# Kernel optimization log

Measured on AMD Instinct MI355X. Metric: run time of the kernel, lower is better.

The kernel has to match this reference:

```python
import jax, jax.numpy as jnp
import numpy as np

B, S, HID = 2, 2048, 4096
NH, NKV, HD = 32, 8, 128
N_REP = NH // NKV
SCALING = HD ** -0.5


def rotate_half(x):
    x1, x2 = x[..., : x.shape[-1] // 2], x[..., x.shape[-1] // 2 :]
    return jnp.concatenate((-x2, x1), axis=-1)


def setup_inputs() -> dict:
    key = jax.random.key(0)
    ks = jax.random.split(key, 8)
    hidden_states = jax.random.normal(ks[0], (B, S, HID), dtype=jnp.float32)
    # rotary embeddings (realistic cos/sin from inverse-frequency angles)
    inv_freq = 1.0 / (10000.0 ** (jnp.arange(0, HD, 2, dtype=jnp.float32) / HD))
    pos = jnp.arange(S, dtype=jnp.float32)
    ang = pos[:, None] * inv_freq[None, :]  # [S, HD/2]
    emb = jnp.concatenate([ang, ang], axis=-1)  # [S, HD]
    cos = jnp.broadcast_to(jnp.cos(emb)[None], (B, S, HD))
    sin = jnp.broadcast_to(jnp.sin(emb)[None], (B, S, HD))
    # additive causal mask [B,1,S,S]
    causal = jnp.triu(jnp.full((S, S), -1e9, dtype=jnp.float32), k=1)
    attention_mask = jnp.broadcast_to(causal[None, None], (B, 1, S, S))
    std = HID ** -0.5
    Wq = jax.random.normal(ks[1], (NH * HD, HID), dtype=jnp.float32) * std
    Wk = jax.random.normal(ks[2], (NKV * HD, HID), dtype=jnp.float32) * std
    Wv = jax.random.normal(ks[3], (NKV * HD, HID), dtype=jnp.float32) * std
    Wo = jax.random.normal(ks[4], (HID, NH * HD), dtype=jnp.float32) * std
    return {"hidden_states": hidden_states, "cos": cos, "sin": sin,
            "attention_mask": attention_mask, "Wq": Wq, "Wk": Wk, "Wv": Wv, "Wo": Wo}


def reference(hidden_states, cos, sin, attention_mask, Wq, Wk, Wv, Wo):
    b, s, _ = hidden_states.shape
    # projections (nn.Linear: x @ W.T), reshape to [B, H, S, D]
    q = (hidden_states @ Wq.T).reshape(b, s, NH, HD).transpose(0, 2, 1, 3)
    k = (hidden_states @ Wk.T).reshape(b, s, NKV, HD).transpose(0, 2, 1, 3)
    v = (hidden_states @ Wv.T).reshape(b, s, NKV, HD).transpose(0, 2, 1, 3)
    # RoPE, cos/sin broadcast over head dim
    c, sn = cos[:, None], sin[:, None]  # [B,1,S,D]
    q = q * c + rotate_half(q) * sn
    k = k * c + rotate_half(k) * sn
    # GQA repeat_kv
    k = jnp.repeat(k, N_REP, axis=1)
    v = jnp.repeat(v, N_REP, axis=1)
    # eager attention
    attn = jnp.einsum("bhqd,bhkd->bhqk", q, k) * SCALING
    attn = attn + attention_mask[:, :, :, : k.shape[2]]
    attn = jax.nn.softmax(attn.astype(jnp.float32), axis=-1).astype(q.dtype)
    out = jnp.einsum("bhqk,bhkd->bhqd", attn, v)
    out = out.transpose(0, 2, 1, 3).reshape(b, s, NH * HD)
    return out @ Wo.T
```

## Files before the change

### kernel.cpp

```cpp
#include <hip/hip_runtime.h>


typedef __bf16 bf16x8 __attribute__((ext_vector_type(8)));
typedef __bf16 bf16x4 __attribute__((ext_vector_type(4)));
typedef float floatx4 __attribute__((ext_vector_type(4)));

#define S_LEN 2048
#define HIDN  4096
#define NH    32
#define NKV   8
#define HD    128

__device__ inline void async_copy16(const void* g, void* l) {
  __builtin_amdgcn_global_load_lds(
      (const __attribute__((address_space(1))) void*)g,
      (__attribute__((address_space(3))) void*)l, 16, 0, 0);
}

template<int N> __device__ __forceinline__ void waitv() {
  static_assert(N == 0 || N == 3 || N == 4 || N == 6 || N == 8, "vmcnt");
  if constexpr (N == 0)      asm volatile("s_waitcnt vmcnt(0)" ::: "memory");
  else if constexpr (N == 3) asm volatile("s_waitcnt vmcnt(3)" ::: "memory");
  else if constexpr (N == 4) asm volatile("s_waitcnt vmcnt(4)" ::: "memory");
  else if constexpr (N == 6) asm volatile("s_waitcnt vmcnt(6)" ::: "memory");
  else                       asm volatile("s_waitcnt vmcnt(8)" ::: "memory");
}

__global__ __launch_bounds__(256) void cvt_bf16(const float* __restrict__ src,
                                                __bf16* __restrict__ dst, int n8)
{
  int i = blockIdx.x * 256 + threadIdx.x;
  if (i >= n8) return;
  const float4* s = (const float4*)src + (size_t)i * 2;
  float4 a = s[0], b = s[1];
  bf16x8 r = {(__bf16)a.x, (__bf16)a.y, (__bf16)a.z, (__bf16)a.w,
              (__bf16)b.x, (__bf16)b.y, (__bf16)b.z, (__bf16)b.w};
  *((bf16x8*)dst + i) = r;
}

template<int MI_REP>
__device__ __forceinline__ void gemm_core(
    const __bf16* __restrict__ A, const __bf16* __restrict__ WB,
    __bf16* lds, int m0, int n0, int tid, floatx4 (&acc)[MI_REP][4])
{
  constexpr int BM       = MI_REP * 32;
  constexpr int A_BYTES  = BM * 64;
  constexpr int STAGE_B  = A_BYTES + 256 * 64;
  constexpr int A_ROUNDS = BM / 128;
  constexpr int LPT      = A_ROUNDS + 2;
  constexpr int NK       = HIDN / 32;

  const int wave = tid >> 6, lane = tid & 63;
  const int quad = lane >> 4, l16 = lane & 15;
  const int wm = wave >> 2, wn = wave & 3;

  size_t a_src[A_ROUNDS], b_src[2];
  #pragma unroll
  for (int ra = 0; ra < A_ROUNDS; ra++) {
    int idx = ra * 512 + tid;
    int row = idx >> 2, qlog = (idx & 3) ^ ((idx >> 3) & 3);
    a_src[ra] = (size_t)(m0 + row) * HIDN + qlog * 8;
  }
  #pragma unroll
  for (int rb = 0; rb < 2; rb++) {
    int idx = rb * 512 + tid;
    int row = idx >> 2, qlog = (idx & 3) ^ ((idx >> 3) & 3);
    b_src[rb] = (size_t)(n0 + row) * HIDN + qlog * 8;
  }
  const int sw   = (quad ^ ((l16 >> 1) & 3)) * 16;
  const int a_rd = (wm * (MI_REP * 16) + l16) * 64 + sw;
  const int b_rd = A_BYTES + (wn * 64 + l16) * 64 + sw;

  #pragma unroll
  for (int mi = 0; mi < MI_REP; mi++)
    #pragma unroll
    for (int ni = 0; ni < 4; ni++) acc[mi][ni] = (floatx4){0.f, 0.f, 0.f, 0.f};

  char* ldsb = (char*)lds;
  auto stage = [&](int kt) {
    char* sb = ldsb + (size_t)(kt & 3) * STAGE_B;
    const __bf16* ak = A  + (size_t)kt * 32;
    const __bf16* bk = WB + (size_t)kt * 32;
    #pragma unroll
    for (int ra = 0; ra < A_ROUNDS; ra++)
      async_copy16(ak + a_src[ra], sb + (ra * 512 + tid) * 16);
    #pragma unroll
    for (int rb = 0; rb < 2; rb++)
      async_copy16(bk + b_src[rb], sb + A_BYTES + (rb * 512 + tid) * 16);
  };

  stage(0); stage(1); stage(2);

  #pragma unroll 4
  for (int kt = 0; kt < NK; kt++) {
    if (kt < NK - 2)       waitv<2 * LPT>();
    else if (kt == NK - 2) waitv<LPT>();
    else                   waitv<0>();
    __builtin_amdgcn_s_barrier();
    asm volatile("" ::: "memory");
    if (kt + 3 < NK) stage(kt + 3);

    const char* sb = ldsb + (size_t)(kt & 3) * STAGE_B;
    bf16x8 bv[4], av[MI_REP];
    #pragma unroll
    for (int ni = 0; ni < 4; ni++)
      bv[ni] = *(const bf16x8*)(sb + b_rd + ni * 1024);
    #pragma unroll
    for (int mi = 0; mi < MI_REP; mi++)
      av[mi] = *(const bf16x8*)(sb + a_rd + mi * 1024);

    __builtin_amdgcn_s_setprio(1);
    #pragma unroll
    for (int mi = 0; mi < MI_REP; mi++)
      #pragma unroll
      for (int ni = 0; ni < 4; ni++)
        acc[mi][ni] = __builtin_amdgcn_mfma_f32_16x16x32_bf16(
            bv[ni], av[mi], acc[mi][ni], 0, 0, 0);
    __builtin_amdgcn_s_setprio(0);
  }
}

__global__ __launch_bounds__(512, 2) void qkv_gemm_bf16(
    const __bf16* __restrict__ A, const __bf16* __restrict__ WB,
    __bf16* __restrict__ Qb, __bf16* __restrict__ Kb, __bf16* __restrict__ Vt)
{
  __shared__ __bf16 lds[4 * (128 + 256) * 32];
  const int tid = threadIdx.x;
  const int m0 = blockIdx.y * 128, n0 = blockIdx.x * 256;
  floatx4 acc[4][4];
  gemm_core<4>(A, WB, lds, m0, n0, tid, acc);

  const int wave = tid >> 6, lane = tid & 63;
  const int quad = lane >> 4, l16 = lane & 15;
  const int wm = wave >> 2, wn = wave & 3;
  #pragma unroll
  for (int mi = 0; mi < 4; mi++) {
    int m = m0 + wm * 64 + mi * 16 + l16;
    int b = m >> 11, s = m & (S_LEN - 1);
    #pragma unroll
    for (int ni = 0; ni < 4; ni++) {
      int nb = n0 + wn * 64 + ni * 16 + quad * 4;
      if (nb < 4096) {
        int hh = nb >> 7, d = nb & 127;
        bf16x4 v = {(__bf16)acc[mi][ni][0], (__bf16)acc[mi][ni][1],
                    (__bf16)acc[mi][ni][2], (__bf16)acc[mi][ni][3]};
        *(bf16x4*)&Qb[(((size_t)b * NH + hh) * S_LEN + s) * HD + d] = v;
      } else if (nb < 5120) {
        int nl = nb - 4096, hh = nl >> 7, d = nl & 127;
        bf16x4 v = {(__bf16)acc[mi][ni][0], (__bf16)acc[mi][ni][1],
                    (__bf16)acc[mi][ni][2], (__bf16)acc[mi][ni][3]};
        *(bf16x4*)&Kb[(((size_t)b * NKV + hh) * S_LEN + s) * HD + d] = v;
      } else {
        int nl = nb - 5120, hh = nl >> 7, d = nl & 127;
        #pragma unroll
        for (int r = 0; r < 4; r++)
          Vt[(((size_t)b * NKV + hh) * HD + d + r) * S_LEN + s] =
              (__bf16)acc[mi][ni][r];
      }
    }
  }
}

__global__ __launch_bounds__(512, 2) void out_gemm_bf16(
    const __bf16* __restrict__ A, const __bf16* __restrict__ WB,
    float* __restrict__ C)
{
  __shared__ __bf16 lds[4 * (256 + 256) * 32];
  const int tid = threadIdx.x;
  const int m0 = blockIdx.y * 256, n0 = blockIdx.x * 256;
  floatx4 acc[8][4];
  gemm_core<8>(A, WB, lds, m0, n0, tid, acc);

  const int wave = tid >> 6, lane = tid & 63;
  const int quad = lane >> 4, l16 = lane & 15;
  const int wm = wave >> 2, wn = wave & 3;
  #pragma unroll
  for (int mi = 0; mi < 8; mi++) {
    int m = m0 + wm * 128 + mi * 16 + l16;
    #pragma unroll
    for (int ni = 0; ni < 4; ni++) {
      int nb = n0 + wn * 64 + ni * 16 + quad * 4;
      *(floatx4*)&C[(size_t)m * HIDN + nb] = acc[mi][ni];
    }
  }
}

__global__ __launch_bounds__(256) void qkv_gemm_f32(
    const float* __restrict__ A, const float* __restrict__ Wq,
    const float* __restrict__ Wk, const float* __restrict__ Wv,
    __bf16* __restrict__ Qb, __bf16* __restrict__ Kb, __bf16* __restrict__ Vt)
{
  __shared__ __bf16 As[128 * 40];
  __shared__ __bf16 Bs[128 * 40];
  const int tid  = threadIdx.x;
  const int wave = tid >> 6, lane = tid & 63;
  const int quad = lane >> 4, l16 = lane & 15;
  const int wrow = (wave >> 1) * 64, wcol = (wave & 1) * 64;
  const int m0 = blockIdx.y * 128;
  const int n0 = blockIdx.x * 128;

  const float* W; int wr0; int sel;
  if (n0 < 4096)      { W = Wq; wr0 = n0;        sel = 0; }
  else if (n0 < 5120) { W = Wk; wr0 = n0 - 4096; sel = 1; }
  else                { W = Wv; wr0 = n0 - 5120; sel = 2; }

  floatx4 acc[4][4];
  #pragma unroll
  for (int i = 0; i < 4; i++)
    #pragma unroll
    for (int j = 0; j < 4; j++) acc[i][j] = (floatx4){0.f, 0.f, 0.f, 0.f};

  for (int k0 = 0; k0 < HIDN; k0 += 32) {
    __syncthreads();
    #pragma unroll
    for (int it = 0; it < 4; ++it) {
      int c = tid + it * 256;
      int row = c >> 3, c4 = (c & 7) * 4;
      float4 va = *(const float4*)(A + (size_t)(m0 + row) * HIDN + k0 + c4);
      __bf16* da = &As[row * 40 + c4];
      da[0] = (__bf16)va.x; da[1] = (__bf16)va.y; da[2] = (__bf16)va.z; da[3] = (__bf16)va.w;
      float4 vb = *(const float4*)(W + (size_t)(wr0 + row) * HIDN + k0 + c4);
      __bf16* db = &Bs[row * 40 + c4];
      db[0] = (__bf16)vb.x; db[1] = (__bf16)vb.y; db[2] = (__bf16)vb.z; db[3] = (__bf16)vb.w;
    }
    __syncthreads();
    bf16x8 af[4], bfr[4];
    #pragma unroll
    for (int i = 0; i < 4; i++)
      af[i] = *(const bf16x8*)&As[(wrow + i * 16 + l16) * 40 + quad * 8];
    #pragma unroll
    for (int j = 0; j < 4; j++)
      bfr[j] = *(const bf16x8*)&Bs[(wcol + j * 16 + l16) * 40 + quad * 8];
    #pragma unroll
    for (int i = 0; i < 4; i++)
      #pragma unroll
      for (int j = 0; j < 4; j++)
        acc[i][j] = __builtin_amdgcn_mfma_f32_16x16x32_bf16(af[i], bfr[j], acc[i][j], 0, 0, 0);
  }

  #pragma unroll
  for (int i = 0; i < 4; i++) {
    #pragma unroll
    for (int j = 0; j < 4; j++) {
      #pragma unroll
      for (int r = 0; r < 4; r++) {
        int m = m0 + wrow + i * 16 + quad * 4 + r;
        int n = n0 + wcol + j * 16 + l16;
        __bf16 v = (__bf16)acc[i][j][r];
        int b = m >> 11, s = m & (S_LEN - 1);
        if (sel == 0) {
          int h = n >> 7, d = n & 127;
          Qb[(((size_t)b * NH + h) * S_LEN + s) * HD + d] = v;
        } else if (sel == 1) {
          int nl = n - 4096, h = nl >> 7, d = nl & 127;
          Kb[(((size_t)b * NKV + h) * S_LEN + s) * HD + d] = v;
        } else {
          int nl = n - 5120, h = nl >> 7, d = nl & 127;
          Vt[(((size_t)b * NKV + h) * HD + d) * S_LEN + s] = v;
        }
      }
    }
  }
}

__global__ __launch_bounds__(256) void out_gemm_f32(
    const __bf16* __restrict__ A, const float* __restrict__ Wo,
    float* __restrict__ C)
{
  __shared__ __bf16 As[128 * 40];
  __shared__ __bf16 Bs[128 * 40];
  const int tid  = threadIdx.x;
  const int wave = tid >> 6, lane = tid & 63;
  const int quad = lane >> 4, l16 = lane & 15;
  const int wrow = (wave >> 1) * 64, wcol = (wave & 1) * 64;
  const int m0 = blockIdx.y * 128;
  const int n0 = blockIdx.x * 128;

  floatx4 acc[4][4];
  #pragma unroll
  for (int i = 0; i < 4; i++)
    #pragma unroll
    for (int j = 0; j < 4; j++) acc[i][j] = (floatx4){0.f, 0.f, 0.f, 0.f};

  for (int k0 = 0; k0 < HIDN; k0 += 32) {
    __syncthreads();
    #pragma unroll
    for (int it = 0; it < 2; ++it) {
      int c = tid + it * 256;
      int row = c >> 2, c8 = (c & 3) * 8;
      *(bf16x8*)&As[row * 40 + c8] =
          *(const bf16x8*)(A + (size_t)(m0 + row) * HIDN + k0 + c8);
    }
    #pragma unroll
    for (int it = 0; it < 4; ++it) {
      int c = tid + it * 256;
      int row = c >> 3, c4 = (c & 7) * 4;
      float4 vb = *(const float4*)(Wo + (size_t)(n0 + row) * HIDN + k0 + c4);
      __bf16* db = &Bs[row * 40 + c4];
      db[0] = (__bf16)vb.x; db[1] = (__bf16)vb.y; db[2] = (__bf16)vb.z; db[3] = (__bf16)vb.w;
    }
    __syncthreads();
    bf16x8 af[4], bfr[4];
    #pragma unroll
    for (int i = 0; i < 4; i++)
      af[i] = *(const bf16x8*)&As[(wrow + i * 16 + l16) * 40 + quad * 8];
    #pragma unroll
    for (int j = 0; j < 4; j++)
      bfr[j] = *(const bf16x8*)&Bs[(wcol + j * 16 + l16) * 40 + quad * 8];
    #pragma unroll
    for (int i = 0; i < 4; i++)
      #pragma unroll
      for (int j = 0; j < 4; j++)
        acc[i][j] = __builtin_amdgcn_mfma_f32_16x16x32_bf16(af[i], bfr[j], acc[i][j], 0, 0, 0);
  }

  #pragma unroll
  for (int i = 0; i < 4; i++)
    #pragma unroll
    for (int j = 0; j < 4; j++)
      #pragma unroll
      for (int r = 0; r < 4; r++) {
        int m = m0 + wrow + i * 16 + quad * 4 + r;
        int n = n0 + wcol + j * 16 + l16;
        C[(size_t)m * HIDN + n] = acc[i][j][r];
      }
}

__global__ __launch_bounds__(256) void rope_kernel(
    __bf16* __restrict__ Qb, __bf16* __restrict__ Kb,
    const float* __restrict__ cosp, const float* __restrict__ sinp)
{
  size_t i = (size_t)blockIdx.x * 256 + threadIdx.x;
  const size_t QP = (size_t)2 * NH * S_LEN * 64;
  __bf16* buf; int H; size_t t;
  if (i < QP) { buf = Qb; H = NH;  t = i; }
  else        { buf = Kb; H = NKV; t = i - QP; }
  int d = (int)(t & 63);
  int s = (int)((t >> 6) & (S_LEN - 1));
  size_t rest = t >> 17;
  int h = (int)(rest % H);
  int b = (int)(rest / H);
  size_t base = (((size_t)b * H + h) * S_LEN + s) * HD;
  float q0 = (float)buf[base + d];
  float q1 = (float)buf[base + d + 64];
  float c  = cosp[((size_t)b * S_LEN + s) * HD + d];
  float sn = sinp[((size_t)b * S_LEN + s) * HD + d];
  buf[base + d]      = (__bf16)(q0 * c - q1 * sn);
  buf[base + d + 64] = (__bf16)(q1 * c + q0 * sn);
}

__global__ __launch_bounds__(256, 2) void flash_attn(
    const __bf16* __restrict__ Q, const __bf16* __restrict__ Kc,
    const __bf16* __restrict__ Vt, __bf16* __restrict__ Out)
{
  __shared__ __bf16 Ks[64 * 136];
  __shared__ __bf16 VTs[128 * 72];
  __shared__ __bf16 Ps[4 * 32 * 72];
  const int tid  = threadIdx.x;
  const int wave = tid >> 6, lane = tid & 63;
  const int quad = lane >> 4, l16 = lane & 15;
  const int bh = blockIdx.x;
  const int h = bh & 31, b = bh >> 5;
  const int qt = 15 - (int)blockIdx.y;
  const int kvh = h >> 2;
  const size_t qbase  = (((size_t)b * NH + h) * S_LEN + qt * 128 + wave * 32) * HD;
  const size_t kbase  = ((size_t)b * NKV + kvh) * S_LEN * HD;
  const size_t vtbase = ((size_t)b * NKV + kvh) * (size_t)HD * S_LEN;
  const int psbase = wave * (32 * 72);

  bf16x8 qf[2][4];
  #pragma unroll
  for (int st = 0; st < 2; st++)
    #pragma unroll
    for (int kk = 0; kk < 4; kk++)
      qf[st][kk] = *(const bf16x8*)&Q[qbase + (size_t)(st * 16 + l16) * HD + kk * 32 + quad * 8];

  floatx4 o[2][8];
  floatx4 ol[2];
  #pragma unroll
  for (int st = 0; st < 2; st++) {
    ol[st] = (floatx4){0.f, 0.f, 0.f, 0.f};
    #pragma unroll
    for (int ct = 0; ct < 8; ct++) o[st][ct] = (floatx4){0.f, 0.f, 0.f, 0.f};
  }
  bf16x8 onesv;
  #pragma unroll
  for (int u = 0; u < 8; u++) onesv[u] = (__bf16)1.0f;

  const float c1 = 0.12753785f;
  const float c2 = -28.853900f;
  const int kj_end = 2 * qt + 2;

  bf16x8 kreg[4], vreg[4];
  #pragma unroll
  for (int it = 0; it < 4; ++it) {
    int c = tid + it * 256;
    kreg[it] = *(const bf16x8*)&Kc[kbase + (size_t)((c >> 4)) * HD + (c & 15) * 8];
    vreg[it] = *(const bf16x8*)&Vt[vtbase + (size_t)(c >> 3) * S_LEN + (c & 7) * 8];
  }

  for (int kj = 0; kj < kj_end; ++kj) {
    __syncthreads();
    #pragma unroll
    for (int it = 0; it < 4; ++it) {
      int c = tid + it * 256;
      *(bf16x8*)&Ks[(c >> 4) * 136 + (c & 15) * 8] = kreg[it];
      *(bf16x8*)&VTs[(c >> 3) * 72 + (c & 7) * 8] = vreg[it];
    }
    __syncthreads();

    if (kj + 1 < kj_end) {
      #pragma unroll
      for (int it = 0; it < 4; ++it) {
        int c = tid + it * 256;
        kreg[it] = *(const bf16x8*)&Kc[kbase + (size_t)((kj + 1) * 64 + (c >> 4)) * HD + (c & 15) * 8];
        vreg[it] = *(const bf16x8*)&Vt[vtbase + (size_t)(c >> 3) * S_LEN + (kj + 1) * 64 + (c & 7) * 8];
      }
    }

    floatx4 s[2][4];
    #pragma unroll
    for (int st = 0; st < 2; st++)
      #pragma unroll
      for (int j = 0; j < 4; j++) s[st][j] = (floatx4){0.f, 0.f, 0.f, 0.f};
    #pragma unroll
    for (int kk = 0; kk < 4; kk++) {
      bf16x8 ak[4];
      #pragma unroll
      for (int j = 0; j < 4; j++)
        ak[j] = *(const bf16x8*)&Ks[(j * 16 + l16) * 136 + kk * 32 + quad * 8];
      #pragma unroll
      for (int st = 0; st < 2; st++)
        #pragma unroll
        for (int j = 0; j < 4; j++)
          s[st][j] = __builtin_amdgcn_mfma_f32_16x16x32_bf16(ak[j], qf[st][kk], s[st][j], 0, 0, 0);
    }

    #pragma unroll
    for (int st = 0; st < 2; st++) {
      const int qrow = qt * 128 + wave * 32 + st * 16 + l16;
      #pragma unroll
      for (int j = 0; j < 4; j++) {
        const int kvb = kj * 64 + j * 16 + quad * 4;
        bf16x4 pw;
        #pragma unroll
        for (int r = 0; r < 4; r++) {
          float p = __builtin_amdgcn_exp2f(fmaf(s[st][j][r], c1, c2));
          if (kvb + r > qrow) p = 0.0f;
          pw[r] = (__bf16)p;
        }
        *(bf16x4*)&Ps[psbase + (st * 16 + l16) * 72 + j * 16 + quad * 4] = pw;
      }
    }

    #pragma unroll
    for (int kk = 0; kk < 2; kk++) {
      bf16x8 bv[8];
      #pragma unroll
      for (int ct = 0; ct < 8; ct++)
        bv[ct] = *(const bf16x8*)&VTs[(ct * 16 + l16) * 72 + kk * 32 + quad * 8];
      #pragma unroll
      for (int st = 0; st < 2; st++) {
        bf16x8 ap = *(const bf16x8*)&Ps[psbase + (st * 16 + l16) * 72 + kk * 32 + quad * 8];
        ol[st] = __builtin_amdgcn_mfma_f32_16x16x32_bf16(ap, onesv, ol[st], 0, 0, 0);
        #pragma unroll
        for (int ct = 0; ct < 8; ct++)
          o[st][ct] = __builtin_amdgcn_mfma_f32_16x16x32_bf16(ap, bv[ct], o[st][ct], 0, 0, 0);
      }
    }
  }

  #pragma unroll
  for (int st = 0; st < 2; st++) {
    #pragma unroll
    for (int r = 0; r < 4; r++) {
      float rl = 1.0f / ol[st][r];
      int qi = qt * 128 + wave * 32 + st * 16 + quad * 4 + r;
      #pragma unroll
      for (int ct = 0; ct < 8; ct++) {
        Out[((size_t)b * S_LEN + qi) * HIDN + h * HD + ct * 16 + l16] =
            (__bf16)(o[st][ct][r] * rl);
      }
    }
  }
}

extern "C" void kernel_launch(void* const* d_in, const int* in_sizes, int n_in,
                              void* d_out, int out_size, void* d_ws, size_t ws_size,
                              hipStream_t stream)
{
  const float* hs   = (const float*)d_in[0];
  const float* cosp = (const float*)d_in[1];
  const float* sinp = (const float*)d_in[2];
  const float* Wq   = (const float*)d_in[4];
  const float* Wk   = (const float*)d_in[5];
  const float* Wv   = (const float*)d_in[6];
  const float* Wo   = (const float*)d_in[7];
  float* out = (float*)d_out;

  __bf16* Qb  = (__bf16*)d_ws;
  __bf16* Kb  = Qb  + (size_t)16777216;
  __bf16* Vtb = Kb  + (size_t)4194304;

  if (ws_size >= (size_t)134217728) {
    __bf16* HSB = Vtb + (size_t)4194304;
    __bf16* AO  = HSB;
    __bf16* WB  = HSB + (size_t)16777216;

    cvt_bf16<<<8192, 256, 0, stream>>>(hs, HSB, 2097152);
    cvt_bf16<<<8192, 256, 0, stream>>>(Wq, WB, 2097152);
    cvt_bf16<<<2048, 256, 0, stream>>>(Wk, WB + 16777216, 524288);
    cvt_bf16<<<2048, 256, 0, stream>>>(Wv, WB + 20971520, 524288);
    qkv_gemm_bf16<<<dim3(24, 32), 512, 0, stream>>>(HSB, WB, Qb, Kb, Vtb);
    cvt_bf16<<<8192, 256, 0, stream>>>(Wo, WB, 2097152);
    rope_kernel<<<40960, 256, 0, stream>>>(Qb, Kb, cosp, sinp);
    flash_attn<<<dim3(64, 16), 256, 0, stream>>>(Qb, Kb, Vtb, AO);
    out_gemm_bf16<<<dim3(16, 16), 512, 0, stream>>>(AO, WB, out);
  } else {
    __bf16* AO = Vtb + (size_t)4194304;
    qkv_gemm_f32<<<dim3(48, 32), 256, 0, stream>>>(hs, Wq, Wk, Wv, Qb, Kb, Vtb);
    rope_kernel<<<40960, 256, 0, stream>>>(Qb, Kb, cosp, sinp);
    flash_attn<<<dim3(64, 16), 256, 0, stream>>>(Qb, Kb, Vtb, AO);
    out_gemm_f32<<<dim3(32, 32), 256, 0, stream>>>(AO, Wo, out);
  }
}
```

Before: 672.9 us.

## Use BK=64 triple-buffered GEMM core, smaller out-proj tile, setprio in attention

Replaces the BK=32 four-stage GEMM core with a BK=64 three-stage ring buffer. It uses a new XOR swizzle over 8 chunks, and each barrier now covers twice as many MFMAs. The output projection switches from 256x256 tiles to 128x256, doubling its grid so more workgroups fill the CUs. The flash-attention inner loops hoist the P-fragment loads and wrap their MFMA blocks in s_setprio. The aim is fewer barriers and waits per unit of K and better occupancy, at the cost of more LDS per stage and less reuse per output-GEMM tile.

```diff
diff --git a/kernel.cpp b/kernel.cpp
--- a/kernel.cpp
+++ b/kernel.cpp
@@ -18,12 +18,9 @@
 }
 
 template<int N> __device__ __forceinline__ void waitv() {
-  static_assert(N == 0 || N == 3 || N == 4 || N == 6 || N == 8, "vmcnt");
-  if constexpr (N == 0)      asm volatile("s_waitcnt vmcnt(0)" ::: "memory");
-  else if constexpr (N == 3) asm volatile("s_waitcnt vmcnt(3)" ::: "memory");
-  else if constexpr (N == 4) asm volatile("s_waitcnt vmcnt(4)" ::: "memory");
-  else if constexpr (N == 6) asm volatile("s_waitcnt vmcnt(6)" ::: "memory");
-  else                       asm volatile("s_waitcnt vmcnt(8)" ::: "memory");
+  static_assert(N == 0 || N == 6, "vmcnt");
+  if constexpr (N == 0) asm volatile("s_waitcnt vmcnt(0)" ::: "memory");
+  else                  asm volatile("s_waitcnt vmcnt(6)" ::: "memory");
 }
 
 __global__ __launch_bounds__(256) void cvt_bf16(const float* __restrict__ src,
@@ -38,85 +35,90 @@
   *((bf16x8*)dst + i) = r;
 }
 
-template<int MI_REP>
-__device__ __forceinline__ void gemm_core(
+__device__ __forceinline__ void gemm_core64(
     const __bf16* __restrict__ A, const __bf16* __restrict__ WB,
-    __bf16* lds, int m0, int n0, int tid, floatx4 (&acc)[MI_REP][4])
-{
-  constexpr int BM       = MI_REP * 32;
-  constexpr int A_BYTES  = BM * 64;
-  constexpr int STAGE_B  = A_BYTES + 256 * 64;
-  constexpr int A_ROUNDS = BM / 128;
-  constexpr int LPT      = A_ROUNDS + 2;
-  constexpr int NK       = HIDN / 32;
+    __bf16* lds, int m0, int n0, int tid, floatx4 (&acc)[4][4])
+{
+  constexpr int A_BYTES = 128 * 64 * 2;
+  constexpr int STAGE_B = (128 + 256) * 64 * 2;
+  constexpr int NK      = HIDN / 64;
 
   const int wave = tid >> 6, lane = tid & 63;
   const int quad = lane >> 4, l16 = lane & 15;
   const int wm = wave >> 2, wn = wave & 3;
 
-  size_t a_src[A_ROUNDS], b_src[2];
-  #pragma unroll
-  for (int ra = 0; ra < A_ROUNDS; ra++) {
+  size_t a_src[2], b_src[4];
+  #pragma unroll
+  for (int ra = 0; ra < 2; ra++) {
     int idx = ra * 512 + tid;
-    int row = idx >> 2, qlog = (idx & 3) ^ ((idx >> 3) & 3);
-    a_src[ra] = (size_t)(m0 + row) * HIDN + qlog * 8;
-  }
-  #pragma unroll
-  for (int rb = 0; rb < 2; rb++) {
+    int row = idx >> 3, chunk = (idx & 7) ^ (row & 7);
+    a_src[ra] = (size_t)(m0 + row) * HIDN + chunk * 8;
+  }
+  #pragma unroll
+  for (int rb = 0; rb < 4; rb++) {
     int idx = rb * 512 + tid;
-    int row = idx >> 2, qlog = (idx & 3) ^ ((idx >> 3) & 3);
-    b_src[rb] = (size_t)(n0 + row) * HIDN + qlog * 8;
-  }
-  const int sw   = (quad ^ ((l16 >> 1) & 3)) * 16;
-  const int a_rd = (wm * (MI_REP * 16) + l16) * 64 + sw;
-  const int b_rd = A_BYTES + (wn * 64 + l16) * 64 + sw;
-
-  #pragma unroll
-  for (int mi = 0; mi < MI_REP; mi++)
+    int row = idx >> 3, chunk = (idx & 7) ^ (row & 7);
+    b_src[rb] = (size_t)(n0 + row) * HIDN + chunk * 8;
+  }
+
+  const int swq  = (quad ^ (l16 & 3)) * 16;
+  const int kxor = ((l16 >> 2) & 1) * 64;
+  const int a_rd = (wm * 64 + l16) * 128 + swq;
+  const int b_rd = A_BYTES + (wn * 64 + l16) * 128 + swq;
+
+  #pragma unroll
+  for (int mi = 0; mi < 4; mi++)
     #pragma unroll
     for (int ni = 0; ni < 4; ni++) acc[mi][ni] = (floatx4){0.f, 0.f, 0.f, 0.f};
 
   char* ldsb = (char*)lds;
-  auto stage = [&](int kt) {
-    char* sb = ldsb + (size_t)(kt & 3) * STAGE_B;
-    const __bf16* ak = A  + (size_t)kt * 32;
-    const __bf16* bk = WB + (size_t)kt * 32;
-    #pragma unroll
-    for (int ra = 0; ra < A_ROUNDS; ra++)
-      async_copy16(ak + a_src[ra], sb + (ra * 512 + tid) * 16);
-    #pragma unroll
-    for (int rb = 0; rb < 2; rb++)
-      async_copy16(bk + b_src[rb], sb + A_BYTES + (rb * 512 + tid) * 16);
+  auto stage = [&](int kt, int slotB) {
+    char* sb = ldsb + slotB;
+    const size_t ko = (size_t)kt * 64;
+    #pragma unroll
+    for (int ra = 0; ra < 2; ra++)
+      async_copy16(A + ko + a_src[ra], sb + (ra * 512 + tid) * 16);
+    #pragma unroll
+    for (int rb = 0; rb < 4; rb++)
+      async_copy16(WB + ko + b_src[rb], sb + A_BYTES + (rb * 512 + tid) * 16);
   };
 
-  stage(0); stage(1); stage(2);
-
-  #pragma unroll 4
+  stage(0, 0);
+  stage(1, STAGE_B);
+
+  int sco = 0, spo = 2 * STAGE_B;
   for (int kt = 0; kt < NK; kt++) {
-    if (kt < NK - 2)       waitv<2 * LPT>();
-    else if (kt == NK - 2) waitv<LPT>();
-    else                   waitv<0>();
+    if (kt < NK - 1) waitv<6>();
+    else             waitv<0>();
     __builtin_amdgcn_s_barrier();
     asm volatile("" ::: "memory");
-    if (kt + 3 < NK) stage(kt + 3);
-
-    const char* sb = ldsb + (size_t)(kt & 3) * STAGE_B;
-    bf16x8 bv[4], av[MI_REP];
-    #pragma unroll
-    for (int ni = 0; ni < 4; ni++)
-      bv[ni] = *(const bf16x8*)(sb + b_rd + ni * 1024);
-    #pragma unroll
-    for (int mi = 0; mi < MI_REP; mi++)
-      av[mi] = *(const bf16x8*)(sb + a_rd + mi * 1024);
-
+    if (kt + 2 < NK) stage(kt + 2, spo);
+
+    const char* sb = ldsb + sco;
+    bf16x8 av[4][2], bv[4][2];
+    #pragma unroll
+    for (int kk = 0; kk < 2; kk++) {
+      const int kb = (kk << 6) ^ kxor;
+      #pragma unroll
+      for (int ni = 0; ni < 4; ni++)
+        bv[ni][kk] = *(const bf16x8*)(sb + b_rd + ni * 2048 + kb);
+      #pragma unroll
+      for (int mi = 0; mi < 4; mi++)
+        av[mi][kk] = *(const bf16x8*)(sb + a_rd + mi * 2048 + kb);
+    }
     __builtin_amdgcn_s_setprio(1);
     #pragma unroll
-    for (int mi = 0; mi < MI_REP; mi++)
-      #pragma unroll
-      for (int ni = 0; ni < 4; ni++)
-        acc[mi][ni] = __builtin_amdgcn_mfma_f32_16x16x32_bf16(
-            bv[ni], av[mi], acc[mi][ni], 0, 0, 0);
+    for (int kk = 0; kk < 2; kk++)
+      #pragma unroll
+      for (int mi = 0; mi < 4; mi++)
+        #pragma unroll
+        for (int ni = 0; ni < 4; ni++)
+          acc[mi][ni] = __builtin_amdgcn_mfma_f32_16x16x32_bf16(
+              bv[ni][kk], av[mi][kk], acc[mi][ni], 0, 0, 0);
     __builtin_amdgcn_s_setprio(0);
+
+    sco += STAGE_B; if (sco == 3 * STAGE_B) sco = 0;
+    spo += STAGE_B; if (spo == 3 * STAGE_B) spo = 0;
   }
 }
 
@@ -124,11 +126,11 @@
     const __bf16* __restrict__ A, const __bf16* __restrict__ WB,
     __bf16* __restrict__ Qb, __bf16* __restrict__ Kb, __bf16* __restrict__ Vt)
 {
-  __shared__ __bf16 lds[4 * (128 + 256) * 32];
+  __shared__ __bf16 lds[3 * (128 + 256) * 32 * 2];
   const int tid = threadIdx.x;
   const int m0 = blockIdx.y * 128, n0 = blockIdx.x * 256;
   floatx4 acc[4][4];
-  gemm_core<4>(A, WB, lds, m0, n0, tid, acc);
+  gemm_core64(A, WB, lds, m0, n0, tid, acc);
 
   const int wave = tid >> 6, lane = tid & 63;
   const int quad = lane >> 4, l16 = lane & 15;
@@ -165,18 +167,18 @@
     const __bf16* __restrict__ A, const __bf16* __restrict__ WB,
     float* __restrict__ C)
 {
-  __shared__ __bf16 lds[4 * (256 + 256) * 32];
+  __shared__ __bf16 lds[3 * (128 + 256) * 32 * 2];
   const int tid = threadIdx.x;
-  const int m0 = blockIdx.y * 256, n0 = blockIdx.x * 256;
-  floatx4 acc[8][4];
-  gemm_core<8>(A, WB, lds, m0, n0, tid, acc);
+  const int m0 = blockIdx.y * 128, n0 = blockIdx.x * 256;
+  floatx4 acc[4][4];
+  gemm_core64(A, WB, lds, m0, n0, tid, acc);
 
   const int wave = tid >> 6, lane = tid & 63;
   const int quad = lane >> 4, l16 = lane & 15;
   const int wm = wave >> 2, wn = wave & 3;
   #pragma unroll
-  for (int mi = 0; mi < 8; mi++) {
-    int m = m0 + wm * 128 + mi * 16 + l16;
+  for (int mi = 0; mi < 4; mi++) {
+    int m = m0 + wm * 64 + mi * 16 + l16;
     #pragma unroll
     for (int ni = 0; ni < 4; ni++) {
       int nb = n0 + wn * 64 + ni * 16 + quad * 4;
@@ -429,11 +431,13 @@
       #pragma unroll
       for (int j = 0; j < 4; j++)
         ak[j] = *(const bf16x8*)&Ks[(j * 16 + l16) * 136 + kk * 32 + quad * 8];
+      __builtin_amdgcn_s_setprio(1);
       #pragma unroll
       for (int st = 0; st < 2; st++)
         #pragma unroll
         for (int j = 0; j < 4; j++)
           s[st][j] = __builtin_amdgcn_mfma_f32_16x16x32_bf16(ak[j], qf[st][kk], s[st][j], 0, 0, 0);
+      __builtin_amdgcn_s_setprio(0);
     }
 
     #pragma unroll
@@ -459,14 +463,19 @@
       #pragma unroll
       for (int ct = 0; ct < 8; ct++)
         bv[ct] = *(const bf16x8*)&VTs[(ct * 16 + l16) * 72 + kk * 32 + quad * 8];
+      bf16x8 ap[2];
+      #pragma unroll
+      for (int st = 0; st < 2; st++)
+        ap[st] = *(const bf16x8*)&Ps[psbase + (st * 16 + l16) * 72 + kk * 32 + quad * 8];
+      __builtin_amdgcn_s_setprio(1);
       #pragma unroll
       for (int st = 0; st < 2; st++) {
-        bf16x8 ap = *(const bf16x8*)&Ps[psbase + (st * 16 + l16) * 72 + kk * 32 + quad * 8];
-        ol[st] = __builtin_amdgcn_mfma_f32_16x16x32_bf16(ap, onesv, ol[st], 0, 0, 0);
+        ol[st] = __builtin_amdgcn_mfma_f32_16x16x32_bf16(ap[st], onesv, ol[st], 0, 0, 0);
         #pragma unroll
         for (int ct = 0; ct < 8; ct++)
-          o[st][ct] = __builtin_amdgcn_mfma_f32_16x16x32_bf16(ap, bv[ct], o[st][ct], 0, 0, 0);
-      }
+          o[st][ct] = __builtin_amdgcn_mfma_f32_16x16x32_bf16(ap[st], bv[ct], o[st][ct], 0, 0, 0);
+      }
+      __builtin_amdgcn_s_setprio(0);
     }
   }
 
@@ -515,7 +524,7 @@
     cvt_bf16<<<8192, 256, 0, stream>>>(Wo, WB, 2097152);
     rope_kernel<<<40960, 256, 0, stream>>>(Qb, Kb, cosp, sinp);
     flash_attn<<<dim3(64, 16), 256, 0, stream>>>(Qb, Kb, Vtb, AO);
-    out_gemm_bf16<<<dim3(16, 16), 512, 0, stream>>>(AO, WB, out);
+    out_gemm_bf16<<<dim3(16, 32), 512, 0, stream>>>(AO, WB, out);
   } else {
     __bf16* AO = Vtb + (size_t)4194304;
     qkv_gemm_f32<<<dim3(48, 32), 256, 0, stream>>>(hs, Wq, Wk, Wv, Qb, Kb, Vtb);
```

Measured after the change: 655.2 us. -2.6%, faster.
